# Kernel tuning notes

Measured on AMD Instinct MI355X. Metric: run time of the kernel, lower is better.

The kernel has to match this reference:

```python
import jax, jax.numpy as jnp
import numpy as np

B, H, S, D, KG = 1, 8, 1024, 64, 10

def setup_inputs() -> dict:
    key = jax.random.key(0)
    ks = jax.random.split(key, 16)
    n = jax.random.normal
    u = jax.random.uniform
    return {
        'Q': n(ks[0], (B, H, S, D), dtype=jnp.float32),
        'K': n(ks[1], (B, H, S, D), dtype=jnp.float32),
        'V': n(ks[2], (B, H, S, D), dtype=jnp.float32),
        'distance_matrix': u(ks[3], (B, H, S, S), dtype=jnp.float32) * 10.0,
        'energy_matrix': u(ks[4], (B, H, S, S), dtype=jnp.float32) * 5.0,
        'mask': jnp.ones((B, H, S, S), dtype=jnp.int32),
        'mu_D': n(ks[5], (KG,), dtype=jnp.float32),
        'sigma_D': u(ks[6], (KG,), dtype=jnp.float32) + 0.5,  # keep sigma positive
        'b_D': n(ks[7], (KG,), dtype=jnp.float32) * 0.1,
        'mu_E': n(ks[8], (KG,), dtype=jnp.float32),
        'sigma_E': u(ks[9], (KG,), dtype=jnp.float32) + 0.5,
        'b_E': n(ks[10], (KG,), dtype=jnp.float32) * 0.1,
        'W1': n(ks[11], (KG, KG), dtype=jnp.float32) / np.sqrt(KG),
        'b1': jnp.zeros((KG,), dtype=jnp.float32),
        'W2': n(ks[12], (1, KG), dtype=jnp.float32) / np.sqrt(KG),
        'b2': jnp.zeros((1,), dtype=jnp.float32),
    }


def _rbf_mlp_bias(x, b, mu, sigma, W1, b1, W2, b2):
    # x: [B,H,S,S] -> Gaussian RBF features over K kernels, then small MLP -> [B,H,S,S]
    z = (x[..., None] + b - mu) / sigma                      # [B,H,S,S,K]
    inv_norm = 1.0 / (jnp.sqrt(2.0 * jnp.pi) * sigma)
    psi = jnp.exp(-0.5 * z * z) * inv_norm                   # [B,H,S,S,K]
    h = jax.nn.gelu(jnp.einsum('bhijk,lk->bhijl', psi, W1) + b1, approximate=False)
    return (jnp.einsum('bhijk,lk->bhijl', h, W2) + b2)[..., 0]


def reference(Q, K, V, distance_matrix, energy_matrix, mask,
              mu_D, sigma_D, b_D, mu_E, sigma_E, b_E, W1, b1, W2, b2):
    d_model = Q.shape[-1]
    scores = jnp.einsum('bhid,bhjd->bhij', Q, K) / np.sqrt(d_model * 2)
    scores = scores + _rbf_mlp_bias(distance_matrix, b_D, mu_D, sigma_D, W1, b1, W2, b2)
    scores = scores + _rbf_mlp_bias(energy_matrix, b_E, mu_E, sigma_E, W1, b1, W2, b2)
    scores = jnp.where(mask == 0, jnp.float32(-1e9), scores)
    attn = jax.nn.softmax(scores, axis=-1)
    return jnp.einsum('bhij,bhjd->bhid', attn, V)
```

## Files before the change

### kernel.cpp

```cpp
#include <hip/hip_runtime.h>
#include <math.h>

#define Hn 8
#define Sn 1024
#define Dn 64
#define KG 10

#define TN 2048
#define RD 10.25f
#define RE 5.125f

typedef __attribute__((ext_vector_type(8))) short bf16x8;
typedef __attribute__((ext_vector_type(4))) float f32x4;
typedef __attribute__((ext_vector_type(4))) _Float16 h16x4;
typedef unsigned short u16;
typedef unsigned int u32;

__device__ inline float bf2f(u16 u) {
    union { u32 i; float f; } v;
    v.i = ((u32)u) << 16;
    return v.f;
}

__device__ inline u16 f2bf(float f) {
    union { float f; u32 i; } v;
    v.f = f;
    u32 i = v.i;
    return (u16)((i + 0x7FFFu + ((i >> 16) & 1u)) >> 16);
}

__device__ inline u16 f2h_bits(float f) {
    union { _Float16 h; u16 u; } cv;
    cv.h = (_Float16)f;
    return cv.u;
}

__device__ float bias_eval(float x,
                           const float* __restrict__ mu, const float* __restrict__ sg,
                           const float* __restrict__ bb,
                           const float* __restrict__ W1, const float* __restrict__ b1,
                           const float* __restrict__ W2, const float* __restrict__ b2) {
    const float inv_s2pi = 0.39894228040143267794f;
    float psi[KG];
#pragma unroll
    for (int k = 0; k < KG; k++) {
        float s = sg[k];
        float z = (x + bb[k] - mu[k]) / s;
        psi[k] = __expf(-0.5f * z * z) * (inv_s2pi / s);
    }
    float out = b2[0];
#pragma unroll
    for (int l = 0; l < KG; l++) {
        float a = b1[l];
#pragma unroll
        for (int k = 0; k < KG; k++) a += psi[k] * W1[l * KG + k];
        float g = 0.5f * a * (1.0f + erff(a * 0.70710678118654752440f));
        out += g * W2[l];
    }
    return out;
}

__global__ __launch_bounds__(256) void build_tables_kernel(
    const float* __restrict__ muD, const float* __restrict__ sgD, const float* __restrict__ bD,
    const float* __restrict__ muE, const float* __restrict__ sgE, const float* __restrict__ bE,
    const float* __restrict__ W1, const float* __restrict__ b1,
    const float* __restrict__ W2, const float* __restrict__ b2,
    u32* __restrict__ tab)
{
    int id = blockIdx.x * 256 + threadIdx.x;
    int which = (id >= TN);
    int idx = id & (TN - 1);
    float h = (which ? RE : RD) / (float)TN;
    float x0 = idx * h;
    float v0, v1;
    if (which) {
        v0 = bias_eval(x0,     muE, sgE, bE, W1, b1, W2, b2);
        v1 = bias_eval(x0 + h, muE, sgE, bE, W1, b1, W2, b2);
    } else {
        v0 = bias_eval(x0,     muD, sgD, bD, W1, b1, W2, b2);
        v1 = bias_eval(x0 + h, muD, sgD, bD, W1, b1, W2, b2);
    }
    tab[id] = (u32)f2bf(v0) | ((u32)f2bf(v1 - v0) << 16);
}

__global__ __launch_bounds__(256) void prep_kernel(
    const float* __restrict__ Q, const float* __restrict__ K, const float* __restrict__ V,
    u16* __restrict__ Qb, u16* __restrict__ Kb, u16* __restrict__ VTi)
{
    __shared__ float tile[64][68];
    const int wg = blockIdx.x, tid = threadIdx.x;

    if (wg < 1024) {
        int i = wg * 256 + tid;
        int arr = i >> 17;
        i &= (1 << 17) - 1;
        float4 v = ((const float4*)(arr ? K : Q))[i];
        ushort4 o;
        o.x = f2bf(v.x); o.y = f2bf(v.y); o.z = f2bf(v.z); o.w = f2bf(v.w);
        ((ushort4*)(arr ? Kb : Qb))[i] = o;
    } else {
        const int b  = wg - 1024;
        const int h  = b >> 4;
        const int s0 = (b & 15) * 64;
        const int rr = tid >> 4, cc = (tid & 15) * 4;
        const float* Vh = V + ((size_t)h * Sn + s0) * Dn;
#pragma unroll
        for (int i = 0; i < 4; i++) {
            float4 v = *(const float4*)(Vh + (size_t)(i * 16 + rr) * Dn + cc);
            tile[i * 16 + rr][cc]     = v.x;
            tile[i * 16 + rr][cc + 1] = v.y;
            tile[i * 16 + rr][cc + 2] = v.z;
            tile[i * 16 + rr][cc + 3] = v.w;
        }
        __syncthreads();
        u16* dst = VTi + (size_t)h * Dn * Sn + s0;
#pragma unroll
        for (int i = 0; i < 4; i++) {
            const int d = i * 16 + rr;
            u16 tmp[4];
#pragma unroll
            for (int j2 = 0; j2 < 4; j2++) {
                int sp = cc + j2;
                int q = (sp >> 3) & 3, j = sp & 7;
                int s = (sp & ~31) + q * 4 + (j & 3) + ((j >> 2) << 4);
                tmp[j2] = f2bf(tile[s][d]);
            }
            ushort4 o = {tmp[0], tmp[1], tmp[2], tmp[3]};
            *(ushort4*)(dst + (size_t)d * Sn + cc) = o;
        }
    }
}

__global__ __launch_bounds__(256, 4) void attn_kernel(
    const u16* __restrict__ Qb, const u16* __restrict__ Kb, const u16* __restrict__ VTi,
    const float* __restrict__ Dm, const float* __restrict__ Em, const int* __restrict__ Mk,
    const u32* __restrict__ gtab, float* __restrict__ out)
{
    __shared__ u16 sBias[16][1032];
    __shared__ union {
        u32 tab[2 * TN];
        struct { float O[4][16][68]; float L[4][16]; } f;
    } sU;

    const int tid  = threadIdx.x;
    const int h    = blockIdx.y;
    const int q0   = blockIdx.x * 16;

    {
        const uint4* g4 = (const uint4*)gtab;
        uint4* s4 = (uint4*)sU.tab;
#pragma unroll
        for (int i = 0; i < 4; i++) s4[tid + 256 * i] = g4[tid + 256 * i];
    }
    __syncthreads();

    {
        const float invhD = (float)TN / RD;
        const float invhE = (float)TN / RE;
        const int prow = tid >> 4;
        const int pcb  = (tid & 15) * 4;
        const size_t roff = ((size_t)h * Sn + q0 + prow) * Sn + pcb;
        const float* Dr = Dm + roff;
        const float* Er = Em + roff;
        const int*   Mr = Mk + roff;

#pragma unroll 4
        for (int i = 0; i < 16; i++) {
            const int c = pcb + i * 64;
            const float4 d4 = *(const float4*)(Dr + i * 64);
            const float4 e4 = *(const float4*)(Er + i * 64);
            const int4   m4 = *(const int4*)(Mr + i * 64);
            const float dv[4] = {d4.x, d4.y, d4.z, d4.w};
            const float ev[4] = {e4.x, e4.y, e4.z, e4.w};
            const int   mv[4] = {m4.x, m4.y, m4.z, m4.w};
            u16 ob[4];
#pragma unroll
            for (int j = 0; j < 4; j++) {
                float tf = dv[j] * invhD;
                int ix = min((int)tf, TN - 1);
                float fr = tf - (float)ix;
                u32 p = sU.tab[ix];
                float vD = fmaf(bf2f((u16)(p >> 16)), fr, bf2f((u16)p));

                tf = ev[j] * invhE;
                ix = min((int)tf, TN - 1);
                fr = tf - (float)ix;
                p = sU.tab[TN + ix];
                float vE = fmaf(bf2f((u16)(p >> 16)), fr, bf2f((u16)p));

                float v = fminf(fmaxf(vD + vE, -60.f), 64.f);
                v = (mv[j] == 0) ? -60.f : v;
                ob[j] = f2h_bits(v);
            }
            *(ushort4*)(&sBias[prow][c]) = *(const ushort4*)ob;
        }
    }
    __syncthreads();

    const int wave = tid >> 6;
    const int lane = tid & 63;
    const int quad = lane >> 4;
    const int l16  = lane & 15;

    const u16* Qh = Qb  + (size_t)h * Sn * Dn;
    const u16* Kh = Kb  + (size_t)h * Sn * Dn;
    const u16* Vh = VTi + (size_t)h * Dn * Sn;
    const float scale = 0.08838834764831845f;

    const bf16x8 bQ0 = *(const bf16x8*)(Qh + (q0 + l16) * Dn + quad * 8);
    const bf16x8 bQ1 = *(const bf16x8*)(Qh + (q0 + l16) * Dn + 32 + quad * 8);

    f32x4 O0 = {0.f, 0.f, 0.f, 0.f}, O1 = O0, O2 = O0, O3 = O0;
    float l_r = 0.f;

    const int kbase = wave * 256;
    const u16* krb = Kh + (size_t)l16 * Dn + quad * 8;
    const u16* vrb = Vh + quad * 8;

    bf16x8 cK[2][4];
    {
        const u16* kr = krb + (size_t)kbase * Dn;
        cK[0][0] = *(const bf16x8*)(kr);
        cK[0][1] = *(const bf16x8*)(kr + 32);
        cK[0][2] = *(const bf16x8*)(kr + 16 * Dn);
        cK[0][3] = *(const bf16x8*)(kr + 16 * Dn + 32);
    }

#pragma unroll
    for (int t = 0; t < 8; t++) {
        const int cur = t & 1, nxt = cur ^ 1;
        const int k0 = kbase + t * 32;

        if (t < 7) {
            const u16* kr = krb + (size_t)(k0 + 32) * Dn;
            cK[nxt][0] = *(const bf16x8*)(kr);
            cK[nxt][1] = *(const bf16x8*)(kr + 32);
            cK[nxt][2] = *(const bf16x8*)(kr + 16 * Dn);
            cK[nxt][3] = *(const bf16x8*)(kr + 16 * Dn + 32);
        }

        const u16* vr = vrb + k0;
        const bf16x8 bV0 = *(const bf16x8*)(vr + (size_t)(l16)      * Sn);
        const bf16x8 bV1 = *(const bf16x8*)(vr + (size_t)(16 + l16) * Sn);
        const bf16x8 bV2 = *(const bf16x8*)(vr + (size_t)(32 + l16) * Sn);
        const bf16x8 bV3 = *(const bf16x8*)(vr + (size_t)(48 + l16) * Sn);

        const h16x4 cb0 = *(const h16x4*)(&sBias[l16][k0 + quad * 4]);
        const h16x4 cb1 = *(const h16x4*)(&sBias[l16][k0 + 16 + quad * 4]);

        f32x4 s0 = {0.f, 0.f, 0.f, 0.f}, s1 = s0;
        s0 = __builtin_amdgcn_mfma_f32_16x16x32_bf16(cK[cur][0], bQ0, s0, 0, 0, 0);
        s0 = __builtin_amdgcn_mfma_f32_16x16x32_bf16(cK[cur][1], bQ1, s0, 0, 0, 0);
        s1 = __builtin_amdgcn_mfma_f32_16x16x32_bf16(cK[cur][2], bQ0, s1, 0, 0, 0);
        s1 = __builtin_amdgcn_mfma_f32_16x16x32_bf16(cK[cur][3], bQ1, s1, 0, 0, 0);

        bf16x8 aP;
#pragma unroll
        for (int r = 0; r < 4; r++) {
            const float p0 = __expf(fmaf(s0[r], scale, (float)cb0[r]));
            const float p1 = __expf(fmaf(s1[r], scale, (float)cb1[r]));
            l_r += p0 + p1;
            aP[r]     = (short)f2bf(p0);
            aP[4 + r] = (short)f2bf(p1);
        }

        O0 = __builtin_amdgcn_mfma_f32_16x16x32_bf16(aP, bV0, O0, 0, 0, 0);
        O1 = __builtin_amdgcn_mfma_f32_16x16x32_bf16(aP, bV1, O1, 0, 0, 0);
        O2 = __builtin_amdgcn_mfma_f32_16x16x32_bf16(aP, bV2, O2, 0, 0, 0);
        O3 = __builtin_amdgcn_mfma_f32_16x16x32_bf16(aP, bV3, O3, 0, 0, 0);
    }

    l_r += __shfl_xor(l_r, 16, 64);
    l_r += __shfl_xor(l_r, 32, 64);
    __syncthreads();
    if (lane < 16) sU.f.L[wave][lane] = l_r;
#pragma unroll
    for (int r = 0; r < 4; r++) {
        sU.f.O[wave][quad * 4 + r][ 0 + l16] = O0[r];
        sU.f.O[wave][quad * 4 + r][16 + l16] = O1[r];
        sU.f.O[wave][quad * 4 + r][32 + l16] = O2[r];
        sU.f.O[wave][quad * 4 + r][48 + l16] = O3[r];
    }
    __syncthreads();

    const int row = tid >> 4;
    const int c4  = (tid & 15) * 4;
    float lg = 0.f;
#pragma unroll
    for (int w = 0; w < 4; w++) lg += sU.f.L[w][row];
    const float inv = 1.0f / lg;

    float acc[4];
#pragma unroll
    for (int c = 0; c < 4; c++) {
        acc[c] = 0.f;
#pragma unroll
        for (int w = 0; w < 4; w++) acc[c] += sU.f.O[w][row][c4 + c];
        acc[c] *= inv;
    }
    float4 ov = {acc[0], acc[1], acc[2], acc[3]};
    *(float4*)(out + ((size_t)(h * Sn + q0 + row)) * Dn + c4) = ov;
}

extern "C" void kernel_launch(void* const* d_in, const int* in_sizes, int n_in,
                              void* d_out, int out_size, void* d_ws, size_t ws_size,
                              hipStream_t stream) {
    const float* Q    = (const float*)d_in[0];
    const float* K    = (const float*)d_in[1];
    const float* V    = (const float*)d_in[2];
    const float* Dm   = (const float*)d_in[3];
    const float* Em   = (const float*)d_in[4];
    const int*   Mask = (const int*)d_in[5];
    const float* muD  = (const float*)d_in[6];
    const float* sgD  = (const float*)d_in[7];
    const float* bD   = (const float*)d_in[8];
    const float* muE  = (const float*)d_in[9];
    const float* sgE  = (const float*)d_in[10];
    const float* bE   = (const float*)d_in[11];
    const float* W1   = (const float*)d_in[12];
    const float* b1   = (const float*)d_in[13];
    const float* W2   = (const float*)d_in[14];
    const float* b2   = (const float*)d_in[15];

    u32* tab = (u32*)d_ws;
    u16* Qb  = (u16*)((char*)d_ws + 2 * TN * 4);
    u16* Kb  = Qb + (size_t)Hn * Sn * Dn;
    u16* VTi = Kb + (size_t)Hn * Sn * Dn;

    build_tables_kernel<<<2 * TN / 256, 256, 0, stream>>>(
        muD, sgD, bD, muE, sgE, bE, W1, b1, W2, b2, tab);

    prep_kernel<<<1152, 256, 0, stream>>>(Q, K, V, Qb, Kb, VTi);

    dim3 grid(Sn / 16, Hn);
    attn_kernel<<<grid, 256, 0, stream>>>(Qb, Kb, VTi, Dm, Em, Mask, tab,
                                          (float*)d_out);
}
```

Measured before the change: 179.2 us.

## Split attention keys across blocks and fuse bias lookup into softmax loop

Splits the key dimension into two halves across a third grid axis, each block writing unnormalized partial outputs and row sums that a new combine kernel sums and normalizes. The shared-memory bias staging pass is removed: distance, energy and mask values are now loaded per tile straight from global memory (distance and energy double-buffered), and the table lookup is done inline just before the exponent. K is no longer prefetched into registers. This aims to double the number of blocks, cut shared memory use, and overlap the large bias-matrix reads with MFMA work, at the cost of an extra kernel launch and partial-buffer traffic. Softmax still omits max subtraction and relies on the clamped bias.

```diff
diff --git a/kernel.cpp b/kernel.cpp
--- a/kernel.cpp
+++ b/kernel.cpp
@@ -5,6 +5,7 @@
 #define Sn 1024
 #define Dn 64
 #define KG 10
+#define KS 2
 
 #define TN 2048
 #define RD 10.25f
@@ -12,7 +13,6 @@
 
 typedef __attribute__((ext_vector_type(8))) short bf16x8;
 typedef __attribute__((ext_vector_type(4))) float f32x4;
-typedef __attribute__((ext_vector_type(4))) _Float16 h16x4;
 typedef unsigned short u16;
 typedef unsigned int u32;
 
@@ -27,12 +27,6 @@
     v.f = f;
     u32 i = v.i;
     return (u16)((i + 0x7FFFu + ((i >> 16) & 1u)) >> 16);
-}
-
-__device__ inline u16 f2h_bits(float f) {
-    union { _Float16 h; u16 u; } cv;
-    cv.h = (_Float16)f;
-    return cv.u;
 }
 
 __device__ float bias_eval(float x,
@@ -131,21 +125,18 @@
     }
 }
 
-__global__ __launch_bounds__(256, 4) void attn_kernel(
+__global__ __launch_bounds__(256, 4) void attn_part_kernel(
     const u16* __restrict__ Qb, const u16* __restrict__ Kb, const u16* __restrict__ VTi,
     const float* __restrict__ Dm, const float* __restrict__ Em, const int* __restrict__ Mk,
-    const u32* __restrict__ gtab, float* __restrict__ out)
+    const u32* __restrict__ gtab,
+    float* __restrict__ Opart, float* __restrict__ Lpart)
 {
-    __shared__ u16 sBias[16][1032];
     __shared__ union {
         u32 tab[2 * TN];
         struct { float O[4][16][68]; float L[4][16]; } f;
     } sU;
 
-    const int tid  = threadIdx.x;
-    const int h    = blockIdx.y;
-    const int q0   = blockIdx.x * 16;
-
+    const int tid = threadIdx.x;
     {
         const uint4* g4 = (const uint4*)gtab;
         uint4* s4 = (uint4*)sU.tab;
@@ -154,49 +145,10 @@
     }
     __syncthreads();
 
-    {
-        const float invhD = (float)TN / RD;
-        const float invhE = (float)TN / RE;
-        const int prow = tid >> 4;
-        const int pcb  = (tid & 15) * 4;
-        const size_t roff = ((size_t)h * Sn + q0 + prow) * Sn + pcb;
-        const float* Dr = Dm + roff;
-        const float* Er = Em + roff;
-        const int*   Mr = Mk + roff;
-
-#pragma unroll 4
-        for (int i = 0; i < 16; i++) {
-            const int c = pcb + i * 64;
-            const float4 d4 = *(const float4*)(Dr + i * 64);
-            const float4 e4 = *(const float4*)(Er + i * 64);
-            const int4   m4 = *(const int4*)(Mr + i * 64);
-            const float dv[4] = {d4.x, d4.y, d4.z, d4.w};
-            const float ev[4] = {e4.x, e4.y, e4.z, e4.w};
-            const int   mv[4] = {m4.x, m4.y, m4.z, m4.w};
-            u16 ob[4];
-#pragma unroll
-            for (int j = 0; j < 4; j++) {
-                float tf = dv[j] * invhD;
-                int ix = min((int)tf, TN - 1);
-                float fr = tf - (float)ix;
-                u32 p = sU.tab[ix];
-                float vD = fmaf(bf2f((u16)(p >> 16)), fr, bf2f((u16)p));
-
-                tf = ev[j] * invhE;
-                ix = min((int)tf, TN - 1);
-                fr = tf - (float)ix;
-                p = sU.tab[TN + ix];
-                float vE = fmaf(bf2f((u16)(p >> 16)), fr, bf2f((u16)p));
-
-                float v = fminf(fmaxf(vD + vE, -60.f), 64.f);
-                v = (mv[j] == 0) ? -60.f : v;
-                ob[j] = f2h_bits(v);
-            }
-            *(ushort4*)(&sBias[prow][c]) = *(const ushort4*)ob;
-        }
-    }
-    __syncthreads();
-
+    const int qb   = blockIdx.x;
+    const int h    = blockIdx.y;
+    const int ks   = blockIdx.z;
+    const int q0   = qb * 16;
     const int wave = tid >> 6;
     const int lane = tid & 63;
     const int quad = lane >> 4;
@@ -205,6 +157,13 @@
     const u16* Qh = Qb  + (size_t)h * Sn * Dn;
     const u16* Kh = Kb  + (size_t)h * Sn * Dn;
     const u16* Vh = VTi + (size_t)h * Dn * Sn;
+    const size_t rowoff = ((size_t)h * Sn + q0 + l16) * Sn;
+    const float* Dr = Dm + rowoff;
+    const float* Er = Em + rowoff;
+    const int*   Mr = Mk + rowoff;
+
+    const float invhD = (float)TN / RD;
+    const float invhE = (float)TN / RE;
     const float scale = 0.08838834764831845f;
 
     const bf16x8 bQ0 = *(const bf16x8*)(Qh + (q0 + l16) * Dn + quad * 8);
@@ -213,31 +172,40 @@
     f32x4 O0 = {0.f, 0.f, 0.f, 0.f}, O1 = O0, O2 = O0, O3 = O0;
     float l_r = 0.f;
 
-    const int kbase = wave * 256;
+    const int kbase = ks * (Sn / KS) + wave * 128;
     const u16* krb = Kh + (size_t)l16 * Dn + quad * 8;
     const u16* vrb = Vh + quad * 8;
 
-    bf16x8 cK[2][4];
+    float4 pD0[2], pD1[2], pE0[2], pE1[2];
     {
-        const u16* kr = krb + (size_t)kbase * Dn;
-        cK[0][0] = *(const bf16x8*)(kr);
-        cK[0][1] = *(const bf16x8*)(kr + 32);
-        cK[0][2] = *(const bf16x8*)(kr + 16 * Dn);
-        cK[0][3] = *(const bf16x8*)(kr + 16 * Dn + 32);
-    }
-
-#pragma unroll
-    for (int t = 0; t < 8; t++) {
+        const int c = kbase + quad * 4;
+        pD0[0] = *(const float4*)(Dr + c);
+        pD1[0] = *(const float4*)(Dr + c + 16);
+        pE0[0] = *(const float4*)(Er + c);
+        pE1[0] = *(const float4*)(Er + c + 16);
+    }
+
+#pragma unroll
+    for (int t = 0; t < 4; t++) {
         const int cur = t & 1, nxt = cur ^ 1;
         const int k0 = kbase + t * 32;
 
-        if (t < 7) {
-            const u16* kr = krb + (size_t)(k0 + 32) * Dn;
-            cK[nxt][0] = *(const bf16x8*)(kr);
-            cK[nxt][1] = *(const bf16x8*)(kr + 32);
-            cK[nxt][2] = *(const bf16x8*)(kr + 16 * Dn);
-            cK[nxt][3] = *(const bf16x8*)(kr + 16 * Dn + 32);
+        if (t < 3) {
+            const int c = k0 + 32 + quad * 4;
+            pD0[nxt] = *(const float4*)(Dr + c);
+            pD1[nxt] = *(const float4*)(Dr + c + 16);
+            pE0[nxt] = *(const float4*)(Er + c);
+            pE1[nxt] = *(const float4*)(Er + c + 16);
         }
+
+        const int4 m0 = *(const int4*)(Mr + k0 + quad * 4);
+        const int4 m1 = *(const int4*)(Mr + k0 + 16 + quad * 4);
+
+        const u16* kr = krb + (size_t)k0 * Dn;
+        const bf16x8 aK00 = *(const bf16x8*)(kr);
+        const bf16x8 aK01 = *(const bf16x8*)(kr + 32);
+        const bf16x8 aK10 = *(const bf16x8*)(kr + 16 * Dn);
+        const bf16x8 aK11 = *(const bf16x8*)(kr + 16 * Dn + 32);
 
         const u16* vr = vrb + k0;
         const bf16x8 bV0 = *(const bf16x8*)(vr + (size_t)(l16)      * Sn);
@@ -245,23 +213,51 @@
         const bf16x8 bV2 = *(const bf16x8*)(vr + (size_t)(32 + l16) * Sn);
         const bf16x8 bV3 = *(const bf16x8*)(vr + (size_t)(48 + l16) * Sn);
 
-        const h16x4 cb0 = *(const h16x4*)(&sBias[l16][k0 + quad * 4]);
-        const h16x4 cb1 = *(const h16x4*)(&sBias[l16][k0 + 16 + quad * 4]);
-
         f32x4 s0 = {0.f, 0.f, 0.f, 0.f}, s1 = s0;
-        s0 = __builtin_amdgcn_mfma_f32_16x16x32_bf16(cK[cur][0], bQ0, s0, 0, 0, 0);
-        s0 = __builtin_amdgcn_mfma_f32_16x16x32_bf16(cK[cur][1], bQ1, s0, 0, 0, 0);
-        s1 = __builtin_amdgcn_mfma_f32_16x16x32_bf16(cK[cur][2], bQ0, s1, 0, 0, 0);
-        s1 = __builtin_amdgcn_mfma_f32_16x16x32_bf16(cK[cur][3], bQ1, s1, 0, 0, 0);
+        s0 = __builtin_amdgcn_mfma_f32_16x16x32_bf16(aK00, bQ0, s0, 0, 0, 0);
+        s0 = __builtin_amdgcn_mfma_f32_16x16x32_bf16(aK01, bQ1, s0, 0, 0, 0);
+        s1 = __builtin_amdgcn_mfma_f32_16x16x32_bf16(aK10, bQ0, s1, 0, 0, 0);
+        s1 = __builtin_amdgcn_mfma_f32_16x16x32_bf16(aK11, bQ1, s1, 0, 0, 0);
+
+        const float dv0[4] = {pD0[cur].x, pD0[cur].y, pD0[cur].z, pD0[cur].w};
+        const float dv1[4] = {pD1[cur].x, pD1[cur].y, pD1[cur].z, pD1[cur].w};
+        const float ev0[4] = {pE0[cur].x, pE0[cur].y, pE0[cur].z, pE0[cur].w};
+        const float ev1[4] = {pE1[cur].x, pE1[cur].y, pE1[cur].z, pE1[cur].w};
+        const int   mv0[4] = {m0.x, m0.y, m0.z, m0.w};
+        const int   mv1[4] = {m1.x, m1.y, m1.z, m1.w};
 
         bf16x8 aP;
 #pragma unroll
         for (int r = 0; r < 4; r++) {
-            const float p0 = __expf(fmaf(s0[r], scale, (float)cb0[r]));
-            const float p1 = __expf(fmaf(s1[r], scale, (float)cb1[r]));
-            l_r += p0 + p1;
-            aP[r]     = (short)f2bf(p0);
-            aP[4 + r] = (short)f2bf(p1);
+            float tf = dv0[r] * invhD;
+            int ix = min((int)tf, TN - 1);
+            u32 p = sU.tab[ix];
+            float b = fmaf(bf2f((u16)(p >> 16)), tf - (float)ix, bf2f((u16)p));
+            tf = ev0[r] * invhE;
+            ix = min((int)tf, TN - 1);
+            p = sU.tab[TN + ix];
+            b += fmaf(bf2f((u16)(p >> 16)), tf - (float)ix, bf2f((u16)p));
+            b = fminf(fmaxf(b, -60.f), 64.f);
+            float v0 = fmaf(s0[r], scale, b);
+            v0 = (mv0[r] == 0) ? -60.f : v0;
+
+            tf = dv1[r] * invhD;
+            ix = min((int)tf, TN - 1);
+            p = sU.tab[ix];
+            b = fmaf(bf2f((u16)(p >> 16)), tf - (float)ix, bf2f((u16)p));
+            tf = ev1[r] * invhE;
+            ix = min((int)tf, TN - 1);
+            p = sU.tab[TN + ix];
+            b += fmaf(bf2f((u16)(p >> 16)), tf - (float)ix, bf2f((u16)p));
+            b = fminf(fmaxf(b, -60.f), 64.f);
+            float v1 = fmaf(s1[r], scale, b);
+            v1 = (mv1[r] == 0) ? -60.f : v1;
+
+            const float e0 = __expf(v0);
+            const float e1 = __expf(v1);
+            l_r += e0 + e1;
+            aP[r]     = (short)f2bf(e0);
+            aP[4 + r] = (short)f2bf(e1);
         }
 
         O0 = __builtin_amdgcn_mfma_f32_16x16x32_bf16(aP, bV0, O0, 0, 0, 0);
@@ -285,10 +281,7 @@
 
     const int row = tid >> 4;
     const int c4  = (tid & 15) * 4;
-    float lg = 0.f;
-#pragma unroll
-    for (int w = 0; w < 4; w++) lg += sU.f.L[w][row];
-    const float inv = 1.0f / lg;
+    const size_t pidx = ((size_t)ks * Hn + h) * (Sn / 16) + qb;
 
     float acc[4];
 #pragma unroll
@@ -296,10 +289,40 @@
         acc[c] = 0.f;
 #pragma unroll
         for (int w = 0; w < 4; w++) acc[c] += sU.f.O[w][row][c4 + c];
-        acc[c] *= inv;
     }
     float4 ov = {acc[0], acc[1], acc[2], acc[3]};
-    *(float4*)(out + ((size_t)(h * Sn + q0 + row)) * Dn + c4) = ov;
+    *(float4*)(Opart + (pidx * 16 + row) * Dn + c4) = ov;
+
+    if ((tid & 15) == 0) {
+        float lg = 0.f;
+#pragma unroll
+        for (int w = 0; w < 4; w++) lg += sU.f.L[w][row];
+        Lpart[pidx * 16 + row] = lg;
+    }
+}
+
+__global__ __launch_bounds__(256) void combine_kernel(
+    const float* __restrict__ Opart, const float* __restrict__ Lpart,
+    float* __restrict__ out)
+{
+    const int qb  = blockIdx.x;
+    const int h   = blockIdx.y;
+    const int tid = threadIdx.x;
+    const int row = tid >> 4;
+    const int c4  = (tid & 15) * 4;
+
+    float acc[4] = {0.f, 0.f, 0.f, 0.f};
+    float lg = 0.f;
+#pragma unroll
+    for (int ks = 0; ks < KS; ks++) {
+        const size_t pidx = ((size_t)ks * Hn + h) * (Sn / 16) + qb;
+        const float4 o = *(const float4*)(Opart + (pidx * 16 + row) * Dn + c4);
+        acc[0] += o.x; acc[1] += o.y; acc[2] += o.z; acc[3] += o.w;
+        lg += Lpart[pidx * 16 + row];
+    }
+    const float inv = 1.0f / lg;
+    float4 ov = {acc[0] * inv, acc[1] * inv, acc[2] * inv, acc[3] * inv};
+    *(float4*)(out + ((size_t)(h * Sn + qb * 16 + row)) * Dn + c4) = ov;
 }
 
 extern "C" void kernel_launch(void* const* d_in, const int* in_sizes, int n_in,
@@ -326,13 +349,18 @@
     u16* Qb  = (u16*)((char*)d_ws + 2 * TN * 4);
     u16* Kb  = Qb + (size_t)Hn * Sn * Dn;
     u16* VTi = Kb + (size_t)Hn * Sn * Dn;
+    float* Opart = (float*)(VTi + (size_t)Hn * Sn * Dn);
+    float* Lpart = Opart + (size_t)KS * Hn * (Sn / 16) * 16 * Dn;
 
     build_tables_kernel<<<2 * TN / 256, 256, 0, stream>>>(
         muD, sgD, bD, muE, sgE, bE, W1, b1, W2, b2, tab);
 
     prep_kernel<<<1152, 256, 0, stream>>>(Q, K, V, Qb, Kb, VTi);
 
-    dim3 grid(Sn / 16, Hn);
-    attn_kernel<<<grid, 256, 0, stream>>>(Qb, Kb, VTi, Dm, Em, Mask, tab,
-                                          (float*)d_out);
-}
+    dim3 grid(Sn / 16, Hn, KS);
+    attn_part_kernel<<<grid, 256, 0, stream>>>(Qb, Kb, VTi, Dm, Em, Mask, tab,
+                                               Opart, Lpart);
+
+    dim3 cgrid(Sn / 16, Hn);
+    combine_kernel<<<cgrid, 256, 0, stream>>>(Opart, Lpart, (float*)d_out);
+}
```

Measured after the change: 181.3 us. About the same (+1.1%).
